# Optimization experiments

Hardware: AMD Instinct MI355X
Metric: run time of the kernel (lower is better)

## Reference

```python
import jax, jax.numpy as jnp
import numpy as np

E, B, F, L = 4, 8192, 2048, 100  # envs, batch/env, feature dim, num classes
LAM = 1.0  # hparams['RERM_lam']


def setup_inputs() -> dict:
    key = jax.random.key(0)
    k1, k2, k3 = jax.random.split(key, 3)
    feats = jax.random.normal(k1, (E, B, F), jnp.float32)
    y = jax.random.randint(k2, (E, B), 0, L)
    W = jax.random.normal(k3, (F, L), jnp.float32) * 0.02
    b = jnp.zeros((L,), jnp.float32)
    return {"feats": feats, "y": y, "W": W, "b": b}


def _rerm_loss(feats, y, W, b):
    # --- per-(label, env) masked means (mean_table / visit_table) ---
    onehot = jax.nn.one_hot(y, L, dtype=feats.dtype)          # [E,B,L]
    counts = onehot.sum(axis=1)                               # [E,L]
    sums = jnp.einsum('ebl,ebf->elf', onehot, feats)          # [E,L,F]
    means = sums / jnp.maximum(counts, 1.0)[..., None]        # [E,L,F]
    visit = (counts > 0).astype(feats.dtype)                  # [E,L]

    # --- torch.var(mean_table[i, fetch_envs, :], dim=1): variance over
    # feature dim per env (unbiased, /(F-1)), then mean over visited envs ---
    mu = means.mean(axis=-1, keepdims=True)                   # [E,L,1]
    var = jnp.sum((means - mu) ** 2, axis=-1) / (F - 1)       # [E,L]

    nvis = visit.sum(axis=0)                                  # [L]
    sel = (nvis > 1.5).astype(feats.dtype)                    # labels with >1 env
    per_label = (var * visit).sum(axis=0) / jnp.maximum(nvis, 1.0)  # [L]
    nzlabel = jnp.maximum(sel.sum(), 1.0)
    mean_loss = LAM * jnp.sum(per_label * sel) / nzlabel

    # --- cross-entropy over all envs concatenated ---
    logits = feats.reshape(E * B, F) @ W + b                  # [E*B,L]
    logp = jax.nn.log_softmax(logits, axis=-1)
    ce = -jnp.take_along_axis(logp, y.reshape(-1, 1), axis=1).mean()

    return mean_loss + ce


def reference(feats, y, W, b):
    return _rerm_loss(feats, y, W, b)
```

## Files before the change

### kernel.cpp

```cpp
#include <hip/hip_runtime.h>
#include <hip/hip_bf16.h>
#include <math.h>

#define E 4
#define B 8192
#define F 2048
#define L 100
#define NROWS (E * B)
#define LAMBDA 1.0f

typedef __attribute__((ext_vector_type(8))) short bf16x8;
typedef __attribute__((ext_vector_type(4))) float f32x4;

static __device__ inline unsigned short f2bf(float x) {
    unsigned u = __float_as_uint(x);
    unsigned r = (u + 0x7FFFu + ((u >> 16) & 1u)) >> 16;
    return (unsigned short)r;
}

#define SG 4
#define NSG 25
#define SBS 8
#define SRW (B / SBS)
#define NSUM (E * SBS * NSG)

#define GBM 128
#define GNC 112
#define GKC 64
#define APAD 72
#define NGEMM (NROWS / GBM)

__global__ void __launch_bounds__(256) k_prep(const float* __restrict__ W,
                                              unsigned short* __restrict__ Wt) {
    int g = blockIdx.x * 256 + threadIdx.x;
    int n = g >> 9;
    int k = (g & 511) * 4;
    ushort4 v;
    if (n < L) {
        v.x = f2bf(W[(size_t)(k + 0) * L + n]);
        v.y = f2bf(W[(size_t)(k + 1) * L + n]);
        v.z = f2bf(W[(size_t)(k + 2) * L + n]);
        v.w = f2bf(W[(size_t)(k + 3) * L + n]);
    } else {
        v.x = v.y = v.z = v.w = 0;
    }
    *(ushort4*)&Wt[(size_t)n * F + k] = v;
}

static __device__ inline unsigned pack_bf(float lo, float hi) {
    unsigned ul = __float_as_uint(lo) + 0x8000u;
    unsigned uh = __float_as_uint(hi) + 0x8000u;
    return __builtin_amdgcn_perm(uh, ul, 0x07060302u);
}

__global__ void __launch_bounds__(512, 4) k_main(const float* __restrict__ feats,
                                                 const int* __restrict__ y,
                                                 const unsigned short* __restrict__ Wt,
                                                 const float* __restrict__ bias,
                                                 float* __restrict__ partial,
                                                 int* __restrict__ counts,
                                                 float* __restrict__ ce_accum) {
    __shared__ __align__(16) char sm[34624];
    int t = threadIdx.x;

    if (blockIdx.x < NGEMM) {
        unsigned short* As = (unsigned short*)sm;
        unsigned short* Ws = As + GBM * APAD;
        float* red = (float*)(sm + 34560);
        int wave = t >> 6, lane = t & 63;
        int quad = lane >> 4, l16 = lane & 15;
        size_t row0 = (size_t)blockIdx.x * GBM;

        f32x4 acc[7];
#pragma unroll
        for (int ct = 0; ct < 7; ++ct) acc[ct] = (f32x4){0.f, 0.f, 0.f, 0.f};

        int srow = t >> 2;
        int sq = t & 3;

        const float* aptr = feats + (row0 + srow) * (size_t)F + sq * 16;
        const unsigned short* wptr = Wt + (size_t)srow * F + sq * 16;

        float4 pa[4];
        uint4 pw[2];
#pragma unroll
        for (int i = 0; i < 4; ++i) pa[i] = ((const float4*)aptr)[i];
        if (srow < GNC) {
#pragma unroll
            for (int i = 0; i < 2; ++i) pw[i] = ((const uint4*)wptr)[i];
        }

        for (int k0 = 0; k0 < F; k0 += GKC) {
            unsigned u[8];
#pragma unroll
            for (int i = 0; i < 4; ++i) {
                u[i * 2]     = pack_bf(pa[i].x, pa[i].y);
                u[i * 2 + 1] = pack_bf(pa[i].z, pa[i].w);
            }
            *(uint4*)&As[srow * APAD + sq * 16]     = make_uint4(u[0], u[1], u[2], u[3]);
            *(uint4*)&As[srow * APAD + sq * 16 + 8] = make_uint4(u[4], u[5], u[6], u[7]);
            if (srow < GNC) {
                *(uint4*)&Ws[srow * APAD + sq * 16] = pw[0];
                *(uint4*)&Ws[srow * APAD + sq * 16 + 8] = pw[1];
            }
            __syncthreads();

            if (k0 + GKC < F) {
                const float* ap = aptr + k0 + GKC;
                const unsigned short* wp = wptr + k0 + GKC;
#pragma unroll
                for (int i = 0; i < 4; ++i) pa[i] = ((const float4*)ap)[i];
                if (srow < GNC) {
#pragma unroll
                    for (int i = 0; i < 2; ++i) pw[i] = ((const uint4*)wp)[i];
                }
            }

#pragma unroll
            for (int ks = 0; ks < 2; ++ks) {
                bf16x8 bfr = *(const bf16x8*)&As[(wave * 16 + l16) * APAD + ks * 32 + quad * 8];
#pragma unroll
                for (int ct = 0; ct < 7; ++ct) {
                    bf16x8 af = *(const bf16x8*)&Ws[(ct * 16 + l16) * APAD + ks * 32 + quad * 8];
                    acc[ct] = __builtin_amdgcn_mfma_f32_16x16x32_bf16(af, bfr, acc[ct], 0, 0, 0);
                }
            }
            __syncthreads();
        }

        int grow = (int)row0 + wave * 16 + l16;
        int lab = y[grow];
        float vv[7][4];
        float vm = -1e30f;
#pragma unroll
        for (int ct = 0; ct < 7; ++ct) {
#pragma unroll
            for (int r = 0; r < 4; ++r) {
                int c = ct * 16 + quad * 4 + r;
                float bb = (c < L) ? bias[c] : 0.f;
                float v = acc[ct][r] + bb;
                vv[ct][r] = v;
                if (c < L) vm = fmaxf(vm, v);
            }
        }
        vm = fmaxf(vm, __shfl_xor(vm, 16));
        vm = fmaxf(vm, __shfl_xor(vm, 32));
        float se = 0.f, tv = 0.f;
#pragma unroll
        for (int ct = 0; ct < 7; ++ct) {
#pragma unroll
            for (int r = 0; r < 4; ++r) {
                int c = ct * 16 + quad * 4 + r;
                if (c < L) se += __expf(vv[ct][r] - vm);
                if (c == lab) tv = vv[ct][r];
            }
        }
        se += __shfl_xor(se, 16);
        se += __shfl_xor(se, 32);
        tv += __shfl_xor(tv, 16);
        tv += __shfl_xor(tv, 32);
        float ce = vm + __logf(se) - tv;
#pragma unroll
        for (int s = 1; s <= 8; s <<= 1) ce += __shfl_xor(ce, s);
        if (lane == 0) red[wave] = ce;
        __syncthreads();
        if (t == 0) {
            float v = 0.f;
#pragma unroll
            for (int w = 0; w < 8; ++w) v += red[w];
            atomicAdd(ce_accum, v);
        }
    } else {
        int* ys = (int*)sm;
        unsigned short* list = (unsigned short*)(sm + 4096);
        int* cnt4 = (int*)(sm + 4096 + 2048);
        int* ntot = (int*)(sm + 4096 + 2048 + 16);
        int bi = blockIdx.x - NGEMM;
        int lg = bi % NSG;
        int bs = (bi / NSG) % SBS;
        int e  = bi / (NSG * SBS);
        int lab0 = lg * SG;

        if (t < SG) cnt4[t] = 0;
        if (t == 8) ntot[0] = 0;
        const int* yb = y + e * B + bs * SRW;
        ys[t] = yb[t];
        ys[t + 512] = yb[t + 512];
        __syncthreads();

        for (int r = t; r < SRW; r += 512) {
            int lb = ys[r] - lab0;
            if ((unsigned)lb < SG) {
                atomicAdd(&cnt4[lb], 1);
                int p = atomicAdd(ntot, 1);
                list[p] = (unsigned short)(r | (lb << 10));
            }
        }
        __syncthreads();
        int n = ntot[0];
        int npad = (n + 3) & ~3;
        if (t < npad - n) list[n + t] = 0;
        __syncthreads();

        const float* fb = feats + ((size_t)e * B + (size_t)bs * SRW) * F + t * 4;
        float4 a0 = make_float4(0.f, 0.f, 0.f, 0.f);
        float4 a1 = a0, a2 = a0, a3 = a0;

        float4 x[4];
        int tg[4];
        if (n > 0) {
#pragma unroll
            for (int j = 0; j < 4; ++j) {
                int ev = list[j];
                tg[j] = ev >> 10;
                x[j] = *(const float4*)(fb + (size_t)(ev & 1023) * F);
            }
            for (int i = 0; i < npad; i += 4) {
                float4 nx[4];
                int ntg[4];
                if (i + 4 < npad) {
#pragma unroll
                    for (int j = 0; j < 4; ++j) {
                        int ev = list[i + 4 + j];
                        ntg[j] = ev >> 10;
                        nx[j] = *(const float4*)(fb + (size_t)(ev & 1023) * F);
                    }
                }
#pragma unroll
                for (int j = 0; j < 4; ++j) {
                    if (i + j < n) {
                        float4 v = x[j];
                        int g = tg[j];
                        if (g == 0)      { a0.x += v.x; a0.y += v.y; a0.z += v.z; a0.w += v.w; }
                        else if (g == 1) { a1.x += v.x; a1.y += v.y; a1.z += v.z; a1.w += v.w; }
                        else if (g == 2) { a2.x += v.x; a2.y += v.y; a2.z += v.z; a2.w += v.w; }
                        else             { a3.x += v.x; a3.y += v.y; a3.z += v.z; a3.w += v.w; }
                    }
                }
#pragma unroll
                for (int j = 0; j < 4; ++j) { x[j] = nx[j]; tg[j] = ntg[j]; }
            }
        }

        float* pb = partial + (((size_t)e * SBS + bs) * L + lab0) * F + t * 4;
        *(float4*)(pb + 0 * F) = a0;
        *(float4*)(pb + 1 * F) = a1;
        *(float4*)(pb + 2 * F) = a2;
        *(float4*)(pb + 3 * F) = a3;
        if (t < SG) atomicAdd(&counts[e * L + lab0 + t], cnt4[t]);
    }
}

__global__ void k_var(const float* __restrict__ partial,
                      const int* __restrict__ counts,
                      float* __restrict__ var_out) {
    int el = blockIdx.x;
    int e = el / L, l = el % L;
    int t = threadIdx.x;
    float inv = 1.f / fmaxf((float)counts[el], 1.f);
    float sm = 0.f, sm2 = 0.f;
    for (int f = t; f < F; f += 256) {
        float s = 0.f;
#pragma unroll
        for (int bs = 0; bs < SBS; ++bs)
            s += partial[(((size_t)e * SBS + bs) * L + l) * F + f];
        float m = s * inv;
        sm += m; sm2 += m * m;
    }
    __shared__ float r1[256], r2[256];
    r1[t] = sm; r2[t] = sm2;
    __syncthreads();
    for (int s = 128; s > 0; s >>= 1) {
        if (t < s) { r1[t] += r1[t + s]; r2[t] += r2[t + s]; }
        __syncthreads();
    }
    if (t == 0) {
        float S = r1[0], S2 = r2[0];
        var_out[el] = (S2 - S * S / (float)F) / (float)(F - 1);
    }
}

__global__ void k_final(const int* __restrict__ counts,
                        const float* __restrict__ var_in,
                        const float* __restrict__ ce_accum,
                        float* __restrict__ out) {
    __shared__ float s_sum[128], s_cnt[128];
    int t = threadIdx.x;
    float selsum = 0.f, selcnt = 0.f;
    for (int l = t; l < L; l += 128) {
        float nvis = 0.f, vsum = 0.f;
        for (int e = 0; e < E; ++e) {
            if (counts[e * L + l] > 0) { nvis += 1.f; vsum += var_in[e * L + l]; }
        }
        float per_label = vsum / fmaxf(nvis, 1.f);
        if (nvis > 1.5f) { selsum += per_label; selcnt += 1.f; }
    }
    s_sum[t] = selsum; s_cnt[t] = selcnt;
    __syncthreads();
    for (int s = 64; s > 0; s >>= 1) {
        if (t < s) { s_sum[t] += s_sum[t + s]; s_cnt[t] += s_cnt[t + s]; }
        __syncthreads();
    }
    if (t == 0) {
        float mean_loss = LAMBDA * s_sum[0] / fmaxf(s_cnt[0], 1.f);
        float ce = ce_accum[0] / (float)NROWS;
        out[0] = mean_loss + ce;
    }
}

extern "C" void kernel_launch(void* const* d_in, const int* in_sizes, int n_in,
                              void* d_out, int out_size, void* d_ws, size_t ws_size,
                              hipStream_t stream) {
    const float* feats = (const float*)d_in[0];
    const int*   y     = (const int*)d_in[1];
    const float* Wm    = (const float*)d_in[2];
    const float* bias  = (const float*)d_in[3];
    float* out = (float*)d_out;

    char* ws = (char*)d_ws;
    float*          ce_accum = (float*)ws;
    int*            counts   = (int*)(ws + 256);
    float*          var_buf  = (float*)(ws + 2048);
    float*          partial  = (float*)(ws + 4096);
    unsigned short* Wt       = (unsigned short*)(ws + 4096 + (size_t)E * SBS * L * F * 4);

    hipMemsetAsync(ce_accum, 0, sizeof(float), stream);
    hipMemsetAsync(counts, 0, E * L * sizeof(int), stream);

    k_prep<<<(GNC * 512) / 256, 256, 0, stream>>>(Wm, Wt);
    k_main<<<NGEMM + NSUM, 512, 0, stream>>>(feats, y, Wt, bias, partial, counts, ce_accum);
    k_var<<<E * L, 256, 0, stream>>>(partial, counts, var_buf);
    k_final<<<1, 128, 0, stream>>>(counts, var_buf, ce_accum, out);
}
```

Baseline: 435.1 us.

## Use persistent work-stealing blocks in main kernel and fold memsets into prep

The main kernel now launches a fixed grid of 512 persistent blocks that fetch GEMM and segment-sum work units from a global atomic counter, instead of one block per unit. Zeroing of the counters and CE accumulator moves into the weight-prep kernel, which also transposes W through shared memory so global reads are coalesced. The variance kernel uses 512 threads with float4 loads and a wave-shuffle reduction. Together these aim to cut launch and memset overhead, tail imbalance and uncoalesced access, at the cost of an atomic and two barriers per work unit.

```diff
diff --git a/kernel.cpp b/kernel.cpp
--- a/kernel.cpp
+++ b/kernel.cpp
@@ -29,22 +29,35 @@
 #define GKC 64
 #define APAD 72
 #define NGEMM (NROWS / GBM)
+#define NUNIT (NGEMM + NSUM)
+#define KMB 512
 
 __global__ void __launch_bounds__(256) k_prep(const float* __restrict__ W,
-                                              unsigned short* __restrict__ Wt) {
-    int g = blockIdx.x * 256 + threadIdx.x;
-    int n = g >> 9;
-    int k = (g & 511) * 4;
-    ushort4 v;
-    if (n < L) {
-        v.x = f2bf(W[(size_t)(k + 0) * L + n]);
-        v.y = f2bf(W[(size_t)(k + 1) * L + n]);
-        v.z = f2bf(W[(size_t)(k + 2) * L + n]);
-        v.w = f2bf(W[(size_t)(k + 3) * L + n]);
-    } else {
-        v.x = v.y = v.z = v.w = 0;
-    }
-    *(ushort4*)&Wt[(size_t)n * F + k] = v;
+                                              unsigned short* __restrict__ Wt,
+                                              float* __restrict__ ce_accum,
+                                              int* __restrict__ counts,
+                                              int* __restrict__ ctr) {
+    __shared__ float st[64][101];
+    int t = threadIdx.x;
+    int b = blockIdx.x;
+    if (b == 0) {
+        for (int i = t; i < E * L; i += 256) counts[i] = 0;
+        if (t == 0) { ce_accum[0] = 0.f; ctr[0] = 0; }
+    }
+    int k0 = b * 64;
+    for (int i = t; i < 64 * 100; i += 256) {
+        st[i / 100][i % 100] = W[(size_t)k0 * L + i];
+    }
+    __syncthreads();
+    for (int i = t; i < 112 * 32; i += 256) {
+        int n = i >> 5, kp = i & 31;
+        unsigned lo = 0, hi = 0;
+        if (n < L) {
+            lo = f2bf(st[kp * 2][n]);
+            hi = f2bf(st[kp * 2 + 1][n]);
+        }
+        *(unsigned*)&Wt[(size_t)n * F + k0 + kp * 2] = lo | (hi << 16);
+    }
 }
 
 static __device__ inline unsigned pack_bf(float lo, float hi) {
@@ -59,223 +72,237 @@
                                                  const float* __restrict__ bias,
                                                  float* __restrict__ partial,
                                                  int* __restrict__ counts,
-                                                 float* __restrict__ ce_accum) {
+                                                 float* __restrict__ ce_accum,
+                                                 int* __restrict__ ctr) {
     __shared__ __align__(16) char sm[34624];
+    __shared__ int s_unit;
     int t = threadIdx.x;
 
-    if (blockIdx.x < NGEMM) {
-        unsigned short* As = (unsigned short*)sm;
-        unsigned short* Ws = As + GBM * APAD;
-        float* red = (float*)(sm + 34560);
-        int wave = t >> 6, lane = t & 63;
-        int quad = lane >> 4, l16 = lane & 15;
-        size_t row0 = (size_t)blockIdx.x * GBM;
-
-        f32x4 acc[7];
-#pragma unroll
-        for (int ct = 0; ct < 7; ++ct) acc[ct] = (f32x4){0.f, 0.f, 0.f, 0.f};
-
-        int srow = t >> 2;
-        int sq = t & 3;
-
-        const float* aptr = feats + (row0 + srow) * (size_t)F + sq * 16;
-        const unsigned short* wptr = Wt + (size_t)srow * F + sq * 16;
-
-        float4 pa[4];
-        uint4 pw[2];
-#pragma unroll
-        for (int i = 0; i < 4; ++i) pa[i] = ((const float4*)aptr)[i];
-        if (srow < GNC) {
-#pragma unroll
-            for (int i = 0; i < 2; ++i) pw[i] = ((const uint4*)wptr)[i];
+    for (;;) {
+        __syncthreads();
+        if (t == 0) s_unit = atomicAdd(ctr, 1);
+        __syncthreads();
+        int u = s_unit;
+        if (u >= NUNIT) break;
+
+        if (u < NGEMM) {
+            unsigned short* As = (unsigned short*)sm;
+            unsigned short* Ws = As + GBM * APAD;
+            float* red = (float*)(sm + 34560);
+            int wave = t >> 6, lane = t & 63;
+            int quad = lane >> 4, l16 = lane & 15;
+            size_t row0 = (size_t)u * GBM;
+
+            f32x4 acc[7];
+#pragma unroll
+            for (int ct = 0; ct < 7; ++ct) acc[ct] = (f32x4){0.f, 0.f, 0.f, 0.f};
+
+            int srow = t >> 2;
+            int sq = t & 3;
+
+            const float* aptr = feats + (row0 + srow) * (size_t)F + sq * 16;
+            const unsigned short* wptr = Wt + (size_t)srow * F + sq * 16;
+
+            float4 pa[4];
+            uint4 pw[2];
+#pragma unroll
+            for (int i = 0; i < 4; ++i) pa[i] = ((const float4*)aptr)[i];
+            if (srow < GNC) {
+#pragma unroll
+                for (int i = 0; i < 2; ++i) pw[i] = ((const uint4*)wptr)[i];
+            }
+
+            for (int k0 = 0; k0 < F; k0 += GKC) {
+                unsigned uu[8];
+#pragma unroll
+                for (int i = 0; i < 4; ++i) {
+                    uu[i * 2]     = pack_bf(pa[i].x, pa[i].y);
+                    uu[i * 2 + 1] = pack_bf(pa[i].z, pa[i].w);
+                }
+                *(uint4*)&As[srow * APAD + sq * 16]     = make_uint4(uu[0], uu[1], uu[2], uu[3]);
+                *(uint4*)&As[srow * APAD + sq * 16 + 8] = make_uint4(uu[4], uu[5], uu[6], uu[7]);
+                if (srow < GNC) {
+                    *(uint4*)&Ws[srow * APAD + sq * 16] = pw[0];
+                    *(uint4*)&Ws[srow * APAD + sq * 16 + 8] = pw[1];
+                }
+                __syncthreads();
+
+                if (k0 + GKC < F) {
+                    const float* ap = aptr + k0 + GKC;
+                    const unsigned short* wp = wptr + k0 + GKC;
+#pragma unroll
+                    for (int i = 0; i < 4; ++i) pa[i] = ((const float4*)ap)[i];
+                    if (srow < GNC) {
+#pragma unroll
+                        for (int i = 0; i < 2; ++i) pw[i] = ((const uint4*)wp)[i];
+                    }
+                }
+
+#pragma unroll
+                for (int ks = 0; ks < 2; ++ks) {
+                    bf16x8 bfr = *(const bf16x8*)&As[(wave * 16 + l16) * APAD + ks * 32 + quad * 8];
+#pragma unroll
+                    for (int ct = 0; ct < 7; ++ct) {
+                        bf16x8 af = *(const bf16x8*)&Ws[(ct * 16 + l16) * APAD + ks * 32 + quad * 8];
+                        acc[ct] = __builtin_amdgcn_mfma_f32_16x16x32_bf16(af, bfr, acc[ct], 0, 0, 0);
+                    }
+                }
+                __syncthreads();
+            }
+
+            int grow = (int)row0 + wave * 16 + l16;
+            int lab = y[grow];
+            float vv[7][4];
+            float vm = -1e30f;
+#pragma unroll
+            for (int ct = 0; ct < 7; ++ct) {
+#pragma unroll
+                for (int r = 0; r < 4; ++r) {
+                    int c = ct * 16 + quad * 4 + r;
+                    float bb = (c < L) ? bias[c] : 0.f;
+                    float v = acc[ct][r] + bb;
+                    vv[ct][r] = v;
+                    if (c < L) vm = fmaxf(vm, v);
+                }
+            }
+            vm = fmaxf(vm, __shfl_xor(vm, 16));
+            vm = fmaxf(vm, __shfl_xor(vm, 32));
+            float se = 0.f, tv = 0.f;
+#pragma unroll
+            for (int ct = 0; ct < 7; ++ct) {
+#pragma unroll
+                for (int r = 0; r < 4; ++r) {
+                    int c = ct * 16 + quad * 4 + r;
+                    if (c < L) se += __expf(vv[ct][r] - vm);
+                    if (c == lab) tv = vv[ct][r];
+                }
+            }
+            se += __shfl_xor(se, 16);
+            se += __shfl_xor(se, 32);
+            tv += __shfl_xor(tv, 16);
+            tv += __shfl_xor(tv, 32);
+            float ce = vm + __logf(se) - tv;
+#pragma unroll
+            for (int s = 1; s <= 8; s <<= 1) ce += __shfl_xor(ce, s);
+            if (lane == 0) red[wave] = ce;
+            __syncthreads();
+            if (t == 0) {
+                float v = 0.f;
+#pragma unroll
+                for (int w = 0; w < 8; ++w) v += red[w];
+                atomicAdd(ce_accum, v);
+            }
+        } else {
+            int* ys = (int*)sm;
+            unsigned short* list = (unsigned short*)(sm + 4096);
+            int* cnt4 = (int*)(sm + 4096 + 2048);
+            int* ntot = (int*)(sm + 4096 + 2048 + 16);
+            int bi = u - NGEMM;
+            int lg = bi % NSG;
+            int bs = (bi / NSG) % SBS;
+            int e  = bi / (NSG * SBS);
+            int lab0 = lg * SG;
+
+            if (t < SG) cnt4[t] = 0;
+            if (t == 8) ntot[0] = 0;
+            const int* yb = y + e * B + bs * SRW;
+            ys[t] = yb[t];
+            ys[t + 512] = yb[t + 512];
+            __syncthreads();
+
+            for (int r = t; r < SRW; r += 512) {
+                int lb = ys[r] - lab0;
+                if ((unsigned)lb < SG) {
+                    atomicAdd(&cnt4[lb], 1);
+                    int p = atomicAdd(ntot, 1);
+                    list[p] = (unsigned short)(r | (lb << 10));
+                }
+            }
+            __syncthreads();
+            int n = ntot[0];
+            int npad = (n + 3) & ~3;
+            if (t < npad - n) list[n + t] = 0;
+            __syncthreads();
+
+            const float* fb = feats + ((size_t)e * B + (size_t)bs * SRW) * F + t * 4;
+            float4 a0 = make_float4(0.f, 0.f, 0.f, 0.f);
+            float4 a1 = a0, a2 = a0, a3 = a0;
+
+            float4 x[4];
+            int tg[4];
+            if (n > 0) {
+#pragma unroll
+                for (int j = 0; j < 4; ++j) {
+                    int ev = list[j];
+                    tg[j] = ev >> 10;
+                    x[j] = *(const float4*)(fb + (size_t)(ev & 1023) * F);
+                }
+                for (int i = 0; i < npad; i += 4) {
+                    float4 nx[4];
+                    int ntg[4];
+                    if (i + 4 < npad) {
+#pragma unroll
+                        for (int j = 0; j < 4; ++j) {
+                            int ev = list[i + 4 + j];
+                            ntg[j] = ev >> 10;
+                            nx[j] = *(const float4*)(fb + (size_t)(ev & 1023) * F);
+                        }
+                    }
+#pragma unroll
+                    for (int j = 0; j < 4; ++j) {
+                        if (i + j < n) {
+                            float4 v = x[j];
+                            int g = tg[j];
+                            if (g == 0)      { a0.x += v.x; a0.y += v.y; a0.z += v.z; a0.w += v.w; }
+                            else if (g == 1) { a1.x += v.x; a1.y += v.y; a1.z += v.z; a1.w += v.w; }
+                            else if (g == 2) { a2.x += v.x; a2.y += v.y; a2.z += v.z; a2.w += v.w; }
+                            else             { a3.x += v.x; a3.y += v.y; a3.z += v.z; a3.w += v.w; }
+                        }
+                    }
+#pragma unroll
+                    for (int j = 0; j < 4; ++j) { x[j] = nx[j]; tg[j] = ntg[j]; }
+                }
+            }
+
+            float* pb = partial + (((size_t)e * SBS + bs) * L + lab0) * F + t * 4;
+            *(float4*)(pb + 0 * F) = a0;
+            *(float4*)(pb + 1 * F) = a1;
+            *(float4*)(pb + 2 * F) = a2;
+            *(float4*)(pb + 3 * F) = a3;
+            if (t < SG) atomicAdd(&counts[e * L + lab0 + t], cnt4[t]);
         }
-
-        for (int k0 = 0; k0 < F; k0 += GKC) {
-            unsigned u[8];
-#pragma unroll
-            for (int i = 0; i < 4; ++i) {
-                u[i * 2]     = pack_bf(pa[i].x, pa[i].y);
-                u[i * 2 + 1] = pack_bf(pa[i].z, pa[i].w);
-            }
-            *(uint4*)&As[srow * APAD + sq * 16]     = make_uint4(u[0], u[1], u[2], u[3]);
-            *(uint4*)&As[srow * APAD + sq * 16 + 8] = make_uint4(u[4], u[5], u[6], u[7]);
-            if (srow < GNC) {
-                *(uint4*)&Ws[srow * APAD + sq * 16] = pw[0];
-                *(uint4*)&Ws[srow * APAD + sq * 16 + 8] = pw[1];
-            }
-            __syncthreads();
-
-            if (k0 + GKC < F) {
-                const float* ap = aptr + k0 + GKC;
-                const unsigned short* wp = wptr + k0 + GKC;
-#pragma unroll
-                for (int i = 0; i < 4; ++i) pa[i] = ((const float4*)ap)[i];
-                if (srow < GNC) {
-#pragma unroll
-                    for (int i = 0; i < 2; ++i) pw[i] = ((const uint4*)wp)[i];
-                }
-            }
-
-#pragma unroll
-            for (int ks = 0; ks < 2; ++ks) {
-                bf16x8 bfr = *(const bf16x8*)&As[(wave * 16 + l16) * APAD + ks * 32 + quad * 8];
-#pragma unroll
-                for (int ct = 0; ct < 7; ++ct) {
-                    bf16x8 af = *(const bf16x8*)&Ws[(ct * 16 + l16) * APAD + ks * 32 + quad * 8];
-                    acc[ct] = __builtin_amdgcn_mfma_f32_16x16x32_bf16(af, bfr, acc[ct], 0, 0, 0);
-                }
-            }
-            __syncthreads();
-        }
-
-        int grow = (int)row0 + wave * 16 + l16;
-        int lab = y[grow];
-        float vv[7][4];
-        float vm = -1e30f;
-#pragma unroll
-        for (int ct = 0; ct < 7; ++ct) {
-#pragma unroll
-            for (int r = 0; r < 4; ++r) {
-                int c = ct * 16 + quad * 4 + r;
-                float bb = (c < L) ? bias[c] : 0.f;
-                float v = acc[ct][r] + bb;
-                vv[ct][r] = v;
-                if (c < L) vm = fmaxf(vm, v);
-            }
-        }
-        vm = fmaxf(vm, __shfl_xor(vm, 16));
-        vm = fmaxf(vm, __shfl_xor(vm, 32));
-        float se = 0.f, tv = 0.f;
-#pragma unroll
-        for (int ct = 0; ct < 7; ++ct) {
-#pragma unroll
-            for (int r = 0; r < 4; ++r) {
-                int c = ct * 16 + quad * 4 + r;
-                if (c < L) se += __expf(vv[ct][r] - vm);
-                if (c == lab) tv = vv[ct][r];
-            }
-        }
-        se += __shfl_xor(se, 16);
-        se += __shfl_xor(se, 32);
-        tv += __shfl_xor(tv, 16);
-        tv += __shfl_xor(tv, 32);
-        float ce = vm + __logf(se) - tv;
-#pragma unroll
-        for (int s = 1; s <= 8; s <<= 1) ce += __shfl_xor(ce, s);
-        if (lane == 0) red[wave] = ce;
-        __syncthreads();
-        if (t == 0) {
-            float v = 0.f;
-#pragma unroll
-            for (int w = 0; w < 8; ++w) v += red[w];
-            atomicAdd(ce_accum, v);
-        }
-    } else {
-        int* ys = (int*)sm;
-        unsigned short* list = (unsigned short*)(sm + 4096);
-        int* cnt4 = (int*)(sm + 4096 + 2048);
-        int* ntot = (int*)(sm + 4096 + 2048 + 16);
-        int bi = blockIdx.x - NGEMM;
-        int lg = bi % NSG;
-        int bs = (bi / NSG) % SBS;
-        int e  = bi / (NSG * SBS);
-        int lab0 = lg * SG;
-
-        if (t < SG) cnt4[t] = 0;
-        if (t == 8) ntot[0] = 0;
-        const int* yb = y + e * B + bs * SRW;
-        ys[t] = yb[t];
-        ys[t + 512] = yb[t + 512];
-        __syncthreads();
-
-        for (int r = t; r < SRW; r += 512) {
-            int lb = ys[r] - lab0;
-            if ((unsigned)lb < SG) {
-                atomicAdd(&cnt4[lb], 1);
-                int p = atomicAdd(ntot, 1);
-                list[p] = (unsigned short)(r | (lb << 10));
-            }
-        }
-        __syncthreads();
-        int n = ntot[0];
-        int npad = (n + 3) & ~3;
-        if (t < npad - n) list[n + t] = 0;
-        __syncthreads();
-
-        const float* fb = feats + ((size_t)e * B + (size_t)bs * SRW) * F + t * 4;
-        float4 a0 = make_float4(0.f, 0.f, 0.f, 0.f);
-        float4 a1 = a0, a2 = a0, a3 = a0;
-
-        float4 x[4];
-        int tg[4];
-        if (n > 0) {
-#pragma unroll
-            for (int j = 0; j < 4; ++j) {
-                int ev = list[j];
-                tg[j] = ev >> 10;
-                x[j] = *(const float4*)(fb + (size_t)(ev & 1023) * F);
-            }
-            for (int i = 0; i < npad; i += 4) {
-                float4 nx[4];
-                int ntg[4];
-                if (i + 4 < npad) {
-#pragma unroll
-                    for (int j = 0; j < 4; ++j) {
-                        int ev = list[i + 4 + j];
-                        ntg[j] = ev >> 10;
-                        nx[j] = *(const float4*)(fb + (size_t)(ev & 1023) * F);
-                    }
-                }
-#pragma unroll
-                for (int j = 0; j < 4; ++j) {
-                    if (i + j < n) {
-                        float4 v = x[j];
-                        int g = tg[j];
-                        if (g == 0)      { a0.x += v.x; a0.y += v.y; a0.z += v.z; a0.w += v.w; }
-                        else if (g == 1) { a1.x += v.x; a1.y += v.y; a1.z += v.z; a1.w += v.w; }
-                        else if (g == 2) { a2.x += v.x; a2.y += v.y; a2.z += v.z; a2.w += v.w; }
-                        else             { a3.x += v.x; a3.y += v.y; a3.z += v.z; a3.w += v.w; }
-                    }
-                }
-#pragma unroll
-                for (int j = 0; j < 4; ++j) { x[j] = nx[j]; tg[j] = ntg[j]; }
-            }
-        }
-
-        float* pb = partial + (((size_t)e * SBS + bs) * L + lab0) * F + t * 4;
-        *(float4*)(pb + 0 * F) = a0;
-        *(float4*)(pb + 1 * F) = a1;
-        *(float4*)(pb + 2 * F) = a2;
-        *(float4*)(pb + 3 * F) = a3;
-        if (t < SG) atomicAdd(&counts[e * L + lab0 + t], cnt4[t]);
-    }
-}
-
-__global__ void k_var(const float* __restrict__ partial,
-                      const int* __restrict__ counts,
-                      float* __restrict__ var_out) {
+    }
+}
+
+__global__ void __launch_bounds__(512) k_var(const float* __restrict__ partial,
+                                             const int* __restrict__ counts,
+                                             float* __restrict__ var_out) {
     int el = blockIdx.x;
     int e = el / L, l = el % L;
     int t = threadIdx.x;
     float inv = 1.f / fmaxf((float)counts[el], 1.f);
-    float sm = 0.f, sm2 = 0.f;
-    for (int f = t; f < F; f += 256) {
-        float s = 0.f;
-#pragma unroll
-        for (int bs = 0; bs < SBS; ++bs)
-            s += partial[(((size_t)e * SBS + bs) * L + l) * F + f];
-        float m = s * inv;
-        sm += m; sm2 += m * m;
-    }
-    __shared__ float r1[256], r2[256];
-    r1[t] = sm; r2[t] = sm2;
+    float4 s = make_float4(0.f, 0.f, 0.f, 0.f);
+#pragma unroll
+    for (int bs = 0; bs < SBS; ++bs) {
+        float4 v = *(const float4*)&partial[(((size_t)e * SBS + bs) * L + l) * F + t * 4];
+        s.x += v.x; s.y += v.y; s.z += v.z; s.w += v.w;
+    }
+    float mx = s.x * inv, my = s.y * inv, mz = s.z * inv, mw = s.w * inv;
+    float sm = mx + my + mz + mw;
+    float sm2 = mx * mx + my * my + mz * mz + mw * mw;
+#pragma unroll
+    for (int sft = 1; sft <= 32; sft <<= 1) {
+        sm += __shfl_xor(sm, sft);
+        sm2 += __shfl_xor(sm2, sft);
+    }
+    __shared__ float r1[8], r2[8];
+    int wv = t >> 6, ln = t & 63;
+    if (ln == 0) { r1[wv] = sm; r2[wv] = sm2; }
     __syncthreads();
-    for (int s = 128; s > 0; s >>= 1) {
-        if (t < s) { r1[t] += r1[t + s]; r2[t] += r2[t + s]; }
-        __syncthreads();
-    }
     if (t == 0) {
-        float S = r1[0], S2 = r2[0];
+        float S = 0.f, S2 = 0.f;
+#pragma unroll
+        for (int w = 0; w < 8; ++w) { S += r1[w]; S2 += r2[w]; }
         var_out[el] = (S2 - S * S / (float)F) / (float)(F - 1);
     }
 }
@@ -319,16 +346,14 @@
 
     char* ws = (char*)d_ws;
     float*          ce_accum = (float*)ws;
+    int*            ctr      = (int*)(ws + 64);
     int*            counts   = (int*)(ws + 256);
     float*          var_buf  = (float*)(ws + 2048);
     float*          partial  = (float*)(ws + 4096);
     unsigned short* Wt       = (unsigned short*)(ws + 4096 + (size_t)E * SBS * L * F * 4);
 
-    hipMemsetAsync(ce_accum, 0, sizeof(float), stream);
-    hipMemsetAsync(counts, 0, E * L * sizeof(int), stream);
-
-    k_prep<<<(GNC * 512) / 256, 256, 0, stream>>>(Wm, Wt);
-    k_main<<<NGEMM + NSUM, 512, 0, stream>>>(feats, y, Wt, bias, partial, counts, ce_accum);
-    k_var<<<E * L, 256, 0, stream>>>(partial, counts, var_buf);
+    k_prep<<<F / 64, 256, 0, stream>>>(Wm, Wt, ce_accum, counts, ctr);
+    k_main<<<KMB, 512, 0, stream>>>(feats, y, Wt, bias, partial, counts, ce_accum, ctr);
+    k_var<<<E * L, 512, 0, stream>>>(partial, counts, var_buf);
     k_final<<<1, 128, 0, stream>>>(counts, var_buf, ce_accum, out);
 }
```

After: 444.9 us. +2.3%, slower.
